# Optimization experiments

Hardware: AMD Instinct MI355X
Metric: run time of the kernel (lower is better)

Reference implementation:

```python
import jax, jax.numpy as jnp
import numpy as np

ALPHA = 0.2          # LeakyReLU negative slope
ORTHO_LAMBDA = 0.01  # orthogonal regularization weight


def setup_inputs() -> dict:
    key = jax.random.key(0)
    ks = jax.random.split(key, 9)
    N, IN, OUT, NR, H = 50000, 128, 128, 64, 4
    E1, E2 = 200000, 50000
    return {
        "input": jax.random.normal(ks[0], (N, IN), jnp.float32),
        "edge": jax.random.randint(ks[1], (2, E1), 0, N),
        "edge_embed": jax.random.normal(ks[2], (E1, NR), jnp.float32),
        "edge_list_nhop": jax.random.randint(ks[3], (2, E2), 0, N),
        "edge_embed_nhop": jax.random.normal(ks[4], (E2, NR), jnp.float32),
        "proj": jax.random.normal(ks[5], (H, IN, IN), jnp.float32) / np.sqrt(IN).astype(np.float32),
        "W": jax.random.normal(ks[6], (H, OUT, 2 * IN + NR), jnp.float32) * 0.08,
        "a": jax.random.normal(ks[7], (H, 1, OUT), jnp.float32) * 0.1,
        "head_weights": jnp.ones((H,), jnp.float32),
    }


def reference(input, edge, edge_embed, edge_list_nhop, edge_embed_nhop, proj, W, a, head_weights):
    N, IN = input.shape
    H, OUT, _ = W.shape
    e = jnp.concatenate([edge, edge_list_nhop], axis=1)              # [2, E]
    emb = jnp.concatenate([edge_embed, edge_embed_nhop], axis=0)     # [E, NR]
    src, tgt = e[0], e[1]

    # per-head orthogonal projections: head_input[h] = input @ proj[h].T -> [H, N, IN]
    hin = jnp.einsum('ni,hoi->hno', input, proj)

    # edge_m = W @ concat(h_src, h_tgt, rel) without materializing the concat
    W_src, W_tgt, W_rel = W[:, :, :IN], W[:, :, IN:2 * IN], W[:, :, 2 * IN:]
    edge_m = (jnp.einsum('hei,hoi->heo', hin[:, src, :], W_src)
              + jnp.einsum('hei,hoi->heo', hin[:, tgt, :], W_tgt)
              + jnp.einsum('er,hor->heo', emb, W_rel))               # [H, E, OUT]

    scores = jnp.einsum('heo,ho->he', edge_m, a[:, 0, :])            # [H, E]
    powers = -jnp.where(scores > 0, scores, ALPHA * scores)         # -leakyrelu
    edge_e = jnp.exp(powers)                                         # [H, E]

    seg = lambda v: jax.ops.segment_sum(v, src, num_segments=N)
    e_rowsum = jnp.clip(jax.vmap(seg)(edge_e), 1e-12, None)          # [H, N]

    edge_w = edge_e[:, :, None] * edge_m                             # [H, E, OUT]
    head_out = jax.vmap(seg)(edge_w)                                 # [H, N, OUT]

    w = jax.nn.softmax(head_weights)
    out = jnp.einsum('h,hnd->nd', w, head_out)                       # [N, OUT]
    # faithful to torch: divides by the LAST head's e_rowsum (loop leakage)
    out = out / e_rowsum[-1][:, None]

    pp = jnp.einsum('hij,hkj->hik', proj, proj)                      # proj @ proj.T
    eye = jnp.eye(proj.shape[1], dtype=proj.dtype)
    orth_reg = ORTHO_LAMBDA * jnp.sum(jnp.sqrt(jnp.sum((pp - eye) ** 2, axis=(1, 2))))

    return jax.nn.elu(out), orth_reg
```

## Files before the change

### kernel.cpp

```cpp
#include <hip/hip_runtime.h>
#include <math.h>


#define NHEAD 4

typedef unsigned short u16;
typedef __attribute__((ext_vector_type(4))) unsigned short u16x4;
typedef __attribute__((ext_vector_type(8))) unsigned short u16x8;
typedef __attribute__((ext_vector_type(8))) short bf16x8;
typedef __attribute__((ext_vector_type(4))) float f32x4;

__device__ __forceinline__ float bf2f(u16 v) {
    union { unsigned u; float f; } x; x.u = ((unsigned)v) << 16; return x.f;
}
__device__ __forceinline__ u16 f2bf(float f) {
    union { float f; unsigned u; } x; x.f = f;
    const unsigned r = x.u + 0x7FFFu + ((x.u >> 16) & 1u);
    return (u16)(r >> 16);
}

__global__ __launch_bounds__(256) void k1_prep(
    const float* __restrict__ proj, const float* __restrict__ W,
    const float* __restrict__ a, const float* __restrict__ hw,
    u16* __restrict__ M_bf,
    float* __restrict__ asrc, float* __restrict__ atgt, float* __restrict__ arel,
    u16* __restrict__ WcatT_bf, float* __restrict__ wsoft,
    float* __restrict__ orth_part)
{
    __shared__ float projS[128*132];
    __shared__ float WS[32*132];
    __shared__ float tS[128];
    __shared__ float red[256];
    const int h = blockIdx.x;
    const int part = blockIdx.y;
    const int z = blockIdx.z;
    const int tid = threadIdx.x;
    const float* projH = proj + h*(128*128);
    const float* WH = W + h*(128*320);
    const float* aH = a + h*128;

    {
        const float4* p4 = (const float4*)projH;
        for (int idx = tid; idx < 4096; idx += 256)
            *(float4*)&projS[(idx>>5)*132 + (idx&31)*4] = p4[idx];
    }

    if (part < 2) {
        const int koff = part ? 128 : 0;
        for (int idx = tid; idx < 1024; idx += 256) {
            const int ol = idx>>5, jq = idx&31;
            *(float4*)&WS[ol*132 + jq*4] = *(const float4*)&WH[(z*32+ol)*320 + koff + jq*4];
        }
        __syncthreads();
        u16* Mout = M_bf + ((size_t)(part*4 + h))*16384;
        for (int idx = tid; idx < 1024; idx += 256) {
            const int ol = idx>>5, jq = idx&31;
            float4 acc; acc.x=0.f; acc.y=0.f; acc.z=0.f; acc.w=0.f;
            for (int i = 0; i < 128; ++i) {
                const float wv = WS[ol*132 + i];
                const float4 pv = *(const float4*)&projS[i*132 + jq*4];
                acc.x += wv*pv.x; acc.y += wv*pv.y; acc.z += wv*pv.z; acc.w += wv*pv.w;
            }
            u16x4 pk; pk.x=f2bf(acc.x); pk.y=f2bf(acc.y); pk.z=f2bf(acc.z); pk.w=f2bf(acc.w);
            *(u16x4*)&Mout[(z*32+ol)*128 + jq*4] = pk;
        }
        if (z == 0) {
            if (tid < 128) {
                float s = 0.f;
                for (int o = 0; o < 128; ++o) s += aH[o]*WH[o*320 + koff + tid];
                tS[tid] = s;
            }
            __syncthreads();
            if (tid < 128) {
                float s = 0.f;
                for (int i = 0; i < 128; ++i) s += tS[i]*projS[i*132 + tid];
                (part ? atgt : asrc)[h*128 + tid] = s;
            }
        }
    } else {
        __syncthreads();
        float local = 0.f;
        const int base = z*4096;
        for (int idx = base + tid; idx < base + 4096; idx += 256) {
            const int i = idx>>7, k = idx&127;
            float s = 0.f;
            for (int q = 0; q < 32; ++q) {
                const float4 pi = *(const float4*)&projS[i*132 + q*4];
                const float4 pk = *(const float4*)&projS[k*132 + q*4];
                s += pi.x*pk.x + pi.y*pk.y + pi.z*pk.z + pi.w*pk.w;
            }
            if (i == k) s -= 1.f;
            local += s*s;
        }
        red[tid] = local;
        __syncthreads();
        for (int st = 128; st > 0; st >>= 1) {
            if (tid < st) red[tid] += red[tid+st];
            __syncthreads();
        }
        if (tid == 0) atomicAdd(&orth_part[h], red[0]);
        if (z == 0) {
            if (tid < 64) {
                float s = 0.f;
                for (int o = 0; o < 128; ++o) s += aH[o]*WH[o*320 + 256 + tid];
                arel[h*64 + tid] = s;
            }
            for (int idx = tid; idx < 8192; idx += 256) {
                const int r = idx & 63, o = idx >> 6;
                WcatT_bf[(size_t)o*256 + h*64 + r] = f2bf(WH[o*320 + 256 + r]);
            }
            if (h == 0 && tid == 0) {
                const float m = fmaxf(fmaxf(hw[0],hw[1]), fmaxf(hw[2],hw[3]));
                const float e0=expf(hw[0]-m), e1=expf(hw[1]-m), e2=expf(hw[2]-m), e3=expf(hw[3]-m);
                const float s = e0+e1+e2+e3;
                wsoft[0]=e0/s; wsoft[1]=e1/s; wsoft[2]=e2/s; wsoft[3]=e3/s;
            }
        }
    }
}

__global__ __launch_bounds__(256) void k0_nodes(
    const float* __restrict__ input, const float* __restrict__ asrc, const float* __restrict__ atgt,
    u16* __restrict__ in_bf, float* __restrict__ s_src, float* __restrict__ s_tgt, int N)
{
    __shared__ float aS[512], tS[512];
    const int tid = threadIdx.x;
    for (int idx = tid; idx < 512; idx += 256) { aS[idx] = asrc[idx]; tS[idx] = atgt[idx]; }
    __syncthreads();
    const int n = blockIdx.x*256 + tid;
    if (n >= N) return;
    const float4* inr = (const float4*)(input + (size_t)n*128);
    u16* ob = in_bf + (size_t)n*128;
    float ss[4] = {0.f,0.f,0.f,0.f}, st[4] = {0.f,0.f,0.f,0.f};
    for (int q = 0; q < 32; ++q) {
        const float4 v = inr[q];
        u16x4 pk; pk.x=f2bf(v.x); pk.y=f2bf(v.y); pk.z=f2bf(v.z); pk.w=f2bf(v.w);
        *(u16x4*)(ob + q*4) = pk;
        #pragma unroll
        for (int hh = 0; hh < 4; ++hh) {
            const float4 av = *(const float4*)&aS[hh*128 + q*4];
            const float4 tv = *(const float4*)&tS[hh*128 + q*4];
            ss[hh] += v.x*av.x + v.y*av.y + v.z*av.z + v.w*av.w;
            st[hh] += v.x*tv.x + v.y*tv.y + v.z*tv.z + v.w*tv.w;
        }
    }
    float4 o1; o1.x=ss[0]; o1.y=ss[1]; o1.z=ss[2]; o1.w=ss[3];
    float4 o2; o2.x=st[0]; o2.y=st[1]; o2.z=st[2]; o2.w=st[3];
    *(float4*)(s_src + (size_t)n*4) = o1;
    *(float4*)(s_tgt + (size_t)n*4) = o2;
}

__global__ __launch_bounds__(256) void k2_mfma(
    const u16* __restrict__ in_bf, const u16* __restrict__ M_bf,
    u16* __restrict__ tbl, int N)
{
    __shared__ u16 MS[16384];
    __shared__ u16 DS[128*136];
    const int tid = threadIdx.x;
    const int w = tid >> 6, lane = tid & 63;
    const int mat = blockIdx.y;
    const int n0 = blockIdx.x*256;
    const int m = lane & 15, kg = lane >> 4;

    {
        const u16* Mp = M_bf + (size_t)mat*16384;
        for (int c = tid; c < 2048; c += 256) {
            const int row = c >> 4, c16 = c & 15;
            const u16x8 v = *(const u16x8*)(Mp + row*128 + c16*8);
            *(u16x8*)((char*)MS + row*256 + ((c16*16) ^ ((row&7)<<4))) = v;
        }
    }
    bf16x8 fa[4][4];
    #pragma unroll
    for (int rt = 0; rt < 4; ++rt) {
        int row = n0 + w*64 + rt*16 + m; if (row >= N) row = N-1;
        const u16* ap = in_bf + (size_t)row*128 + kg*8;
        #pragma unroll
        for (int ks = 0; ks < 4; ++ks) fa[rt][ks] = *(const bf16x8*)(ap + ks*32);
    }
    __syncthreads();

    f32x4 acc[4][8];
    #pragma unroll
    for (int rt = 0; rt < 4; ++rt)
        #pragma unroll
        for (int nt = 0; nt < 8; ++nt) { acc[rt][nt][0]=0.f; acc[rt][nt][1]=0.f; acc[rt][nt][2]=0.f; acc[rt][nt][3]=0.f; }

    #pragma unroll
    for (int nt = 0; nt < 8; ++nt) {
        const int o = nt*16 + m;
        bf16x8 fb[4];
        #pragma unroll
        for (int ks = 0; ks < 4; ++ks) {
            const int c16 = kg + 4*ks;
            fb[ks] = *(const bf16x8*)((const char*)MS + o*256 + ((c16*16) ^ ((o&7)<<4)));
        }
        #pragma unroll
        for (int rt = 0; rt < 4; ++rt)
            #pragma unroll
            for (int ks = 0; ks < 4; ++ks)
                acc[rt][nt] = __builtin_amdgcn_mfma_f32_16x16x32_bf16(fa[rt][ks], fb[ks], acc[rt][nt], 0, 0, 0);
    }

    for (int p = 0; p < 2; ++p) {
        __syncthreads();
        if ((w >> 1) == p) {
            #pragma unroll
            for (int rt = 0; rt < 4; ++rt) {
                const int r0 = (w&1)*64 + rt*16 + kg*4;
                #pragma unroll
                for (int nt = 0; nt < 8; ++nt) {
                    const int o = nt*16 + m;
                    #pragma unroll
                    for (int r = 0; r < 4; ++r)
                        DS[(r0+r)*136 + o] = f2bf(acc[rt][nt][r]);
                }
            }
        }
        __syncthreads();
        for (int idx = tid; idx < 2048; idx += 256) {
            const int row = idx >> 4, seg = idx & 15;
            const int n = n0 + p*128 + row;
            if (n < N) {
                const bf16x8 v = *(const bf16x8*)&DS[row*136 + seg*8];
                *(bf16x8*)(tbl + (size_t)n*1024 + mat*128 + seg*8) = v;
            }
        }
    }
}

__global__ __launch_bounds__(256) void k3_edges(
    const int* __restrict__ edge, const int* __restrict__ nhop,
    const float* __restrict__ emb1, const float* __restrict__ emb2,
    const float* __restrict__ s_src, const float* __restrict__ s_tgt,
    const float* __restrict__ arel,
    float* __restrict__ edge_e, int* __restrict__ deg,
    u16* __restrict__ emb_bf, int E1, int E2)
{
    const int tid = threadIdx.x;
    const int g = tid >> 4, l = tid & 15;
    const int E = E1 + E2;
    const float4 ar0 = *(const float4*)(arel + 0*64 + l*4);
    const float4 ar1 = *(const float4*)(arel + 1*64 + l*4);
    const float4 ar2 = *(const float4*)(arel + 2*64 + l*4);
    const float4 ar3 = *(const float4*)(arel + 3*64 + l*4);
    const int ebase = blockIdx.x*256;
    #pragma unroll 4
    for (int it = 0; it < 16; ++it) {
        const int e = ebase + it*16 + g;
        if (e >= E) continue;
        const float4 v = (e < E1) ? *(const float4*)(emb1 + (size_t)e*64 + l*4)
                                  : *(const float4*)(emb2 + (size_t)(e-E1)*64 + l*4);
        u16x4 pk; pk.x=f2bf(v.x); pk.y=f2bf(v.y); pk.z=f2bf(v.z); pk.w=f2bf(v.w);
        *(u16x4*)(emb_bf + (size_t)e*64 + l*4) = pk;
        float p0 = v.x*ar0.x + v.y*ar0.y + v.z*ar0.z + v.w*ar0.w;
        float p1 = v.x*ar1.x + v.y*ar1.y + v.z*ar1.z + v.w*ar1.w;
        float p2 = v.x*ar2.x + v.y*ar2.y + v.z*ar2.z + v.w*ar2.w;
        float p3 = v.x*ar3.x + v.y*ar3.y + v.z*ar3.z + v.w*ar3.w;
        #pragma unroll
        for (int d = 1; d < 16; d <<= 1) {
            p0 += __shfl_xor(p0, d);
            p1 += __shfl_xor(p1, d);
            p2 += __shfl_xor(p2, d);
            p3 += __shfl_xor(p3, d);
        }
        if (l == 0) {
            int src, tgt;
            if (e < E1) { src = edge[e]; tgt = edge[E1+e]; }
            else { const int e2 = e-E1; src = nhop[e2]; tgt = nhop[E2+e2]; }
            const float4 s4 = *(const float4*)(s_src + (size_t)src*4);
            const float4 t4 = *(const float4*)(s_tgt + (size_t)tgt*4);
            float4 eo;
            { const float sc = s4.x+t4.x+p0; eo.x = expf(sc>0.f ? -sc : -0.2f*sc); }
            { const float sc = s4.y+t4.y+p1; eo.y = expf(sc>0.f ? -sc : -0.2f*sc); }
            { const float sc = s4.z+t4.z+p2; eo.z = expf(sc>0.f ? -sc : -0.2f*sc); }
            { const float sc = s4.w+t4.w+p3; eo.w = expf(sc>0.f ? -sc : -0.2f*sc); }
            *(float4*)(edge_e + (size_t)e*4) = eo;
            atomicAdd(&deg[src], 1);
        }
    }
}

__global__ __launch_bounds__(1024) void k_scanA(const int* __restrict__ deg, int* __restrict__ offsets,
                                                int* __restrict__ bsum, int N)
{
    __shared__ int wsumS[16];
    const int tid = threadIdx.x;
    const int lane = tid & 63, wid = tid >> 6;
    const int i0 = blockIdx.x*4096 + tid*4;
    int a0=0,a1=0,a2=0,a3=0;
    if (i0 + 3 < N) { const int4 t = *(const int4*)(deg + i0); a0=t.x; a1=t.y; a2=t.z; a3=t.w; }
    else { if (i0 < N) a0=deg[i0]; if (i0+1 < N) a1=deg[i0+1]; if (i0+2 < N) a2=deg[i0+2]; }
    const int s1=a0+a1, s2=s1+a2, s3=s2+a3;
    int s = s3;
    #pragma unroll
    for (int d = 1; d < 64; d <<= 1) { const int t = __shfl_up(s, d); if (lane >= d) s += t; }
    if (lane == 63) wsumS[wid] = s;
    __syncthreads();
    if (tid < 16) {
        int t = wsumS[tid];
        #pragma unroll
        for (int d = 1; d < 16; d <<= 1) { const int u = __shfl_up(t, d); if (tid >= d) t += u; }
        wsumS[tid] = t;
    }
    __syncthreads();
    const int ex = (wid ? wsumS[wid-1] : 0) + s - s3;
    if (i0 < N)     offsets[i0]   = ex;
    if (i0+1 < N)   offsets[i0+1] = ex + a0;
    if (i0+2 < N)   offsets[i0+2] = ex + s1;
    if (i0+3 < N)   offsets[i0+3] = ex + s2;
    if (tid == 0) bsum[blockIdx.x] = wsumS[15];
}

__global__ __launch_bounds__(64) void k_scanB(const int* __restrict__ bsum, int* __restrict__ boff,
                                              int* __restrict__ offsets, int nb, int N)
{
    const int tid = threadIdx.x;
    const int v = (tid < nb) ? bsum[tid] : 0;
    int s = v;
    #pragma unroll
    for (int d = 1; d < 64; d <<= 1) { const int t = __shfl_up(s, d); if (tid >= d) s += t; }
    if (tid < nb) boff[tid] = s - v;
    if (tid == 63) offsets[N] = s;
}

__global__ __launch_bounds__(256) void k_scanC(int* __restrict__ offsets, const int* __restrict__ boff, int N)
{
    const int i = blockIdx.x*256 + threadIdx.x;
    if (i < N) offsets[i] += boff[i >> 12];
}

__global__ __launch_bounds__(256) void k_fill(
    const int* __restrict__ edge, const int* __restrict__ nhop,
    const float* __restrict__ edge_e,
    const int* __restrict__ offsets, int* __restrict__ cursor,
    int* __restrict__ csr_e, int* __restrict__ csr_tgt, float* __restrict__ ee_perm,
    int E1, int E2)
{
    const int E = E1+E2;
    const int e = blockIdx.x*256 + threadIdx.x;
    if (e >= E) return;
    int src, tgt;
    if (e < E1) { src = edge[e]; tgt = edge[E1+e]; }
    else { const int e2 = e-E1; src = nhop[e2]; tgt = nhop[E2+e2]; }
    const int pos = atomicAdd(&cursor[src], 1);
    const int p = offsets[src] + pos;
    csr_e[p] = e;
    csr_tgt[p] = tgt;
    *(float4*)(ee_perm + (size_t)p*4) = *(const float4*)(edge_e + (size_t)e*4);
}

__global__ __launch_bounds__(256) void k4_gather(
    const float* __restrict__ ee_perm, const int* __restrict__ offsets,
    const int* __restrict__ csr_e, const int* __restrict__ csr_tgt,
    const u16* __restrict__ emb_bf, const u16* __restrict__ tbl,
    const float* __restrict__ wsoft,
    float* __restrict__ pout, u16* __restrict__ semb_bf, float* __restrict__ rowsum3,
    int N)
{
    const int lane = threadIdx.x & 63;
    const int n = blockIdx.x*4 + (threadIdx.x >> 6);
    if (n >= N) return;
    const int hl = lane >> 4;
    const int hoff = hl*128 + (lane & 15)*8;

    union HT { u16x8 v; unsigned u[4]; };

    float acc[8];
    #pragma unroll
    for (int j = 0; j < 8; ++j) acc[j] = 0.f;
    float sm0=0.f, sm1=0.f, sm2=0.f, sm3=0.f;
    float rsl0=0.f, rsl1=0.f, rsl2=0.f, rsl3=0.f;

    const int start = offsets[n], end = offsets[n+1];
    for (int cb = start; cb < end; cb += 64) {
        const int rem = end - cb;
        const int cnt = rem < 64 ? rem : 64;
        int eL = 0, tgtL = 0;
        float4 eeL; eeL.x=0.f; eeL.y=0.f; eeL.z=0.f; eeL.w=0.f;
        if (lane < cnt) {
            eL   = csr_e[cb + lane];
            tgtL = csr_tgt[cb + lane];
            eeL  = *(const float4*)(ee_perm + (size_t)(cb + lane)*4);
        }
        rsl0 += eeL.x; rsl1 += eeL.y; rsl2 += eeL.z; rsl3 += eeL.w;
        const int cp = (cnt + 3) & ~3;

        HT ht0, ht1, ht2, ht3;
        u16 em0, em1, em2, em3;
#define K4_FETCH(J, IDX) { const int tg_ = __shfl(tgtL, (IDX)); const int eg_ = __shfl(eL, (IDX)); \
            ht##J.v = *(const u16x8*)(tbl + (size_t)tg_*1024 + 512 + hoff); \
            em##J = emb_bf[(size_t)eg_*64 + lane]; }
        K4_FETCH(0, 0) K4_FETCH(1, 1) K4_FETCH(2, 2) K4_FETCH(3, 3)

#define K4_STAGE(J) { \
            const float e0 = __shfl(eeL.x, i+J); \
            const float e1 = __shfl(eeL.y, i+J); \
            const float e2 = __shfl(eeL.z, i+J); \
            const float e3 = __shfl(eeL.w, i+J); \
            const float eh = (hl==0)?e0:(hl==1)?e1:(hl==2)?e2:e3; \
            _Pragma("unroll") \
            for (int p = 0; p < 4; ++p) { \
                union{unsigned u; float f;} lo_, hi_; \
                lo_.u = ht##J.u[p] << 16; hi_.u = ht##J.u[p] & 0xffff0000u; \
                acc[2*p]   += eh*lo_.f; \
                acc[2*p+1] += eh*hi_.f; \
            } \
            const float ev = bf2f(em##J); \
            sm0 += e0*ev; sm1 += e1*ev; sm2 += e2*ev; sm3 += e3*ev; \
            { const int ii = i + 4 + J; const int ic = ii < 63 ? ii : 63; K4_FETCH(J, ic) } }

        for (int i = 0; i < cp; i += 4) {
            K4_STAGE(0)
            K4_STAGE(1)
            K4_STAGE(2)
            K4_STAGE(3)
        }
#undef K4_STAGE
#undef K4_FETCH
    }

    #pragma unroll
    for (int d = 1; d < 64; d <<= 1) {
        rsl0 += __shfl_xor(rsl0, d);
        rsl1 += __shfl_xor(rsl1, d);
        rsl2 += __shfl_xor(rsl2, d);
        rsl3 += __shfl_xor(rsl3, d);
    }
    {
        const float rsh = (hl==0)?rsl0:(hl==1)?rsl1:(hl==2)?rsl2:rsl3;
        HT hs; hs.v = *(const u16x8*)(tbl + (size_t)n*1024 + hoff);
        #pragma unroll
        for (int p = 0; p < 4; ++p) {
            union{unsigned u; float f;} lo_, hi_;
            lo_.u = hs.u[p] << 16; hi_.u = hs.u[p] & 0xffff0000u;
            acc[2*p]   += rsh*lo_.f;
            acc[2*p+1] += rsh*hi_.f;
        }
    }
    if (lane == 0) rowsum3[n] = fmaxf(rsl3, 1e-12f);

    const float4 ws4 = *(const float4*)wsoft;
    const float wh = (hl==0)?ws4.x:(hl==1)?ws4.y:(hl==2)?ws4.z:ws4.w;
    float p[8];
    #pragma unroll
    for (int j = 0; j < 8; ++j) {
        float pv = wh*acc[j];
        pv += __shfl_xor(pv, 16);
        pv += __shfl_xor(pv, 32);
        p[j] = pv;
    }
    if (hl == 0) {
        float* op = pout + (size_t)n*128 + (lane & 15)*8;
        float4 A; A.x=p[0]; A.y=p[1]; A.z=p[2]; A.w=p[3];
        float4 B; B.x=p[4]; B.y=p[5]; B.z=p[6]; B.w=p[7];
        *(float4*)op = A;
        *(float4*)(op+4) = B;
    }
    u16* so = semb_bf + (size_t)n*256;
    so[lane]       = f2bf(ws4.x*sm0);
    so[64 + lane]  = f2bf(ws4.y*sm1);
    so[128 + lane] = f2bf(ws4.z*sm2);
    so[192 + lane] = f2bf(ws4.w*sm3);
}

__global__ __launch_bounds__(256) void k5_gemm(
    const u16* __restrict__ semb_bf, const u16* __restrict__ wcatT_bf,
    const float* __restrict__ rowsum3, const float* __restrict__ orth_part,
    float* __restrict__ out, int N)
{
    __shared__ float DS[64*132];
    const int tid = threadIdx.x;
    if (blockIdx.x == 0 && tid == 0)
        out[(size_t)N*128] = 0.01f*(sqrtf(orth_part[0])+sqrtf(orth_part[1])+sqrtf(orth_part[2])+sqrtf(orth_part[3]));
    const int w = tid >> 6, lane = tid & 63;
    const int m = lane & 15, kg = lane >> 4;
    const int n0 = blockIdx.x*64;

    bf16x8 fa[8];
    {
        int row = n0 + w*16 + m; if (row >= N) row = N-1;
        const u16* ap = semb_bf + (size_t)row*256 + kg*8;
        #pragma unroll
        for (int ks = 0; ks < 8; ++ks) fa[ks] = *(const bf16x8*)(ap + ks*32);
    }
    f32x4 acc[8];
    #pragma unroll
    for (int nt = 0; nt < 8; ++nt) { acc[nt][0]=0.f; acc[nt][1]=0.f; acc[nt][2]=0.f; acc[nt][3]=0.f; }
    #pragma unroll
    for (int nt = 0; nt < 8; ++nt) {
        const u16* bp = wcatT_bf + (size_t)(nt*16 + m)*256 + kg*8;
        #pragma unroll
        for (int ks = 0; ks < 8; ++ks) {
            const bf16x8 fb = *(const bf16x8*)(bp + ks*32);
            acc[nt] = __builtin_amdgcn_mfma_f32_16x16x32_bf16(fa[ks], fb, acc[nt], 0, 0, 0);
        }
    }
    #pragma unroll
    for (int nt = 0; nt < 8; ++nt) {
        const int o = nt*16 + m;
        const int r0 = w*16 + kg*4;
        #pragma unroll
        for (int r = 0; r < 4; ++r)
            DS[(r0+r)*132 + o] = acc[nt][r];
    }
    __syncthreads();
    for (int idx = tid; idx < 2048; idx += 256) {
        const int row = idx >> 5, q = idx & 31;
        const int n = n0 + row;
        if (n < N) {
            const float4 d = *(const float4*)&DS[row*132 + q*4];
            float* op = out + (size_t)n*128 + q*4;
            const float4 pv = *(const float4*)op;
            const float rinv = 1.0f / rowsum3[n];
            float v0 = (pv.x + d.x)*rinv;
            float v1 = (pv.y + d.y)*rinv;
            float v2 = (pv.z + d.z)*rinv;
            float v3 = (pv.w + d.w)*rinv;
            v0 = (v0 > 0.f) ? v0 : expm1f(v0);
            v1 = (v1 > 0.f) ? v1 : expm1f(v1);
            v2 = (v2 > 0.f) ? v2 : expm1f(v2);
            v3 = (v3 > 0.f) ? v3 : expm1f(v3);
            float4 r4; r4.x=v0; r4.y=v1; r4.z=v2; r4.w=v3;
            *(float4*)op = r4;
        }
    }
}

extern "C" void kernel_launch(void* const* d_in, const int* in_sizes, int n_in,
                              void* d_out, int out_size, void* d_ws, size_t ws_size,
                              hipStream_t stream)
{
    const float* input = (const float*)d_in[0];
    const int*   edge  = (const int*)d_in[1];
    const float* emb1  = (const float*)d_in[2];
    const int*   nhop  = (const int*)d_in[3];
    const float* emb2  = (const float*)d_in[4];
    const float* proj  = (const float*)d_in[5];
    const float* W     = (const float*)d_in[6];
    const float* a     = (const float*)d_in[7];
    const float* hw    = (const float*)d_in[8];
    float* out = (float*)d_out;

    const int N  = in_sizes[0] / 128;
    const int E1 = in_sizes[1] / 2;
    const int E2 = in_sizes[3] / 2;
    const int E  = E1 + E2;
    (void)n_in; (void)out_size; (void)ws_size;

    char* wsb = (char*)d_ws;
    size_t off = 0;
    auto alloc = [&](size_t bytes) -> char* {
        char* p = wsb + off;
        off += (bytes + 255) & ~(size_t)255;
        return p;
    };
    u16*   in_bf    = (u16*)alloc((size_t)N*128*2);
    u16*   tbl      = (u16*)alloc((size_t)N*1024*2);
    u16*   semb_bf  = (u16*)alloc((size_t)N*256*2);
    u16*   emb_bf   = (u16*)alloc((size_t)E*64*2);
    float* edge_e   = (float*)alloc((size_t)E*4*4);
    float* ee_perm  = (float*)alloc((size_t)E*4*4);
    int*   csr_e    = (int*)alloc((size_t)E*4);
    int*   csr_tgt  = (int*)alloc((size_t)E*4);
    u16*   M_bf     = (u16*)alloc((size_t)8*16384*2);
    u16*   WcatT_bf = (u16*)alloc((size_t)128*256*2);
    float* asrc     = (float*)alloc(512*4);
    float* atgt     = (float*)alloc(512*4);
    float* arel     = (float*)alloc(256*4);
    float* s_src    = (float*)alloc((size_t)N*4*4);
    float* s_tgt    = (float*)alloc((size_t)N*4*4);
    float* wsoft    = (float*)alloc(4*4);
    float* rowsum3  = (float*)alloc((size_t)N*4);
    int*   offsets  = (int*)alloc((size_t)(N+1)*4);
    int*   bsum     = (int*)alloc(64*4);
    int*   boff     = (int*)alloc(64*4);
    const size_t zoff0 = off;
    float* orth_part= (float*)alloc(4*4);
    int*   deg      = (int*)alloc((size_t)N*4);
    int*   cursor   = (int*)alloc((size_t)N*4);
    const size_t zoff1 = off;

    hipMemsetAsync(wsb + zoff0, 0, zoff1 - zoff0, stream);

    const int nbScan = (N + 4095) / 4096;

    k1_prep<<<dim3(NHEAD,3,4), dim3(256), 0, stream>>>(proj, W, a, hw, M_bf,
                                                       asrc, atgt, arel, WcatT_bf, wsoft, orth_part);
    k0_nodes<<<dim3((N+255)/256), dim3(256), 0, stream>>>(input, asrc, atgt, in_bf, s_src, s_tgt, N);
    k2_mfma<<<dim3((N+255)/256, 8), dim3(256), 0, stream>>>(in_bf, M_bf, tbl, N);
    k3_edges<<<dim3((E+255)/256), dim3(256), 0, stream>>>(edge, nhop, emb1, emb2, s_src, s_tgt,
                                                          arel, edge_e, deg, emb_bf, E1, E2);
    k_scanA<<<dim3(nbScan), dim3(1024), 0, stream>>>(deg, offsets, bsum, N);
    k_scanB<<<dim3(1), dim3(64), 0, stream>>>(bsum, boff, offsets, nbScan, N);
    k_scanC<<<dim3((N+255)/256), dim3(256), 0, stream>>>(offsets, boff, N);
    k_fill<<<dim3((E+255)/256), dim3(256), 0, stream>>>(edge, nhop, edge_e, offsets, cursor,
                                                        csr_e, csr_tgt, ee_perm, E1, E2);
    k4_gather<<<dim3((N+3)/4), dim3(256), 0, stream>>>(ee_perm, offsets, csr_e, csr_tgt, emb_bf,
                                                       tbl, wsoft, out, semb_bf, rowsum3, N);
    k5_gemm<<<dim3((N+63)/64), dim3(256), 0, stream>>>(semb_bf, WcatT_bf, rowsum3, orth_part,
                                                       out, N);
}
```

Before: 275.7 us.

## Store gather partials in bf16, fold scan fixup into consumers, swizzle k2 grid

Removes the scanC kernel by adding the per-block scan offset at use sites in k_fill and k4_gather. Writes the k4 partial output as bf16 to a separate buffer rather than fp32 read-modify-write of the output, reducing memory traffic in k4 and k5. Remaps k2 blocks to a 1D swizzled grid and guards gather prefetches by edge count. Trades some precision on the intermediate partial sums.

```diff
diff --git a/kernel.cpp b/kernel.cpp
--- a/kernel.cpp
+++ b/kernel.cpp
@@ -158,8 +158,11 @@
     __shared__ u16 DS[128*136];
     const int tid = threadIdx.x;
     const int w = tid >> 6, lane = tid & 63;
-    const int mat = blockIdx.y;
-    const int n0 = blockIdx.x*256;
+    const int bid = blockIdx.x;
+    const int nx = gridDim.x >> 3;
+    const int swz = (bid & 7)*nx + (bid >> 3);
+    const int n0 = (swz >> 3)*256;
+    const int mat = swz & 7;
     const int m = lane & 15, kg = lane >> 4;
 
     {
@@ -324,16 +327,10 @@
     if (tid == 63) offsets[N] = s;
 }
 
-__global__ __launch_bounds__(256) void k_scanC(int* __restrict__ offsets, const int* __restrict__ boff, int N)
-{
-    const int i = blockIdx.x*256 + threadIdx.x;
-    if (i < N) offsets[i] += boff[i >> 12];
-}
-
 __global__ __launch_bounds__(256) void k_fill(
     const int* __restrict__ edge, const int* __restrict__ nhop,
     const float* __restrict__ edge_e,
-    const int* __restrict__ offsets, int* __restrict__ cursor,
+    const int* __restrict__ offsets, const int* __restrict__ boff, int* __restrict__ cursor,
     int* __restrict__ csr_e, int* __restrict__ csr_tgt, float* __restrict__ ee_perm,
     int E1, int E2)
 {
@@ -344,18 +341,18 @@
     if (e < E1) { src = edge[e]; tgt = edge[E1+e]; }
     else { const int e2 = e-E1; src = nhop[e2]; tgt = nhop[E2+e2]; }
     const int pos = atomicAdd(&cursor[src], 1);
-    const int p = offsets[src] + pos;
+    const int p = offsets[src] + boff[src>>12] + pos;
     csr_e[p] = e;
     csr_tgt[p] = tgt;
     *(float4*)(ee_perm + (size_t)p*4) = *(const float4*)(edge_e + (size_t)e*4);
 }
 
 __global__ __launch_bounds__(256) void k4_gather(
-    const float* __restrict__ ee_perm, const int* __restrict__ offsets,
+    const float* __restrict__ ee_perm, const int* __restrict__ offsets, const int* __restrict__ boff,
     const int* __restrict__ csr_e, const int* __restrict__ csr_tgt,
     const u16* __restrict__ emb_bf, const u16* __restrict__ tbl,
     const float* __restrict__ wsoft,
-    float* __restrict__ pout, u16* __restrict__ semb_bf, float* __restrict__ rowsum3,
+    u16* __restrict__ pout_bf, u16* __restrict__ semb_bf, float* __restrict__ rowsum3,
     int N)
 {
     const int lane = threadIdx.x & 63;
@@ -372,7 +369,8 @@
     float sm0=0.f, sm1=0.f, sm2=0.f, sm3=0.f;
     float rsl0=0.f, rsl1=0.f, rsl2=0.f, rsl3=0.f;
 
-    const int start = offsets[n], end = offsets[n+1];
+    const int start = offsets[n] + boff[n>>12];
+    const int end = (n+1 == N) ? offsets[N] : (offsets[n+1] + boff[(n+1)>>12]);
     for (int cb = start; cb < end; cb += 64) {
         const int rem = end - cb;
         const int cnt = rem < 64 ? rem : 64;
@@ -386,12 +384,16 @@
         rsl0 += eeL.x; rsl1 += eeL.y; rsl2 += eeL.z; rsl3 += eeL.w;
         const int cp = (cnt + 3) & ~3;
 
-        HT ht0, ht1, ht2, ht3;
-        u16 em0, em1, em2, em3;
+        HT zz; zz.u[0]=0u; zz.u[1]=0u; zz.u[2]=0u; zz.u[3]=0u;
+        HT ht0=zz, ht1=zz, ht2=zz, ht3=zz;
+        u16 em0=0, em1=0, em2=0, em3=0;
 #define K4_FETCH(J, IDX) { const int tg_ = __shfl(tgtL, (IDX)); const int eg_ = __shfl(eL, (IDX)); \
             ht##J.v = *(const u16x8*)(tbl + (size_t)tg_*1024 + 512 + hoff); \
             em##J = emb_bf[(size_t)eg_*64 + lane]; }
-        K4_FETCH(0, 0) K4_FETCH(1, 1) K4_FETCH(2, 2) K4_FETCH(3, 3)
+        if (0 < cnt) K4_FETCH(0, 0)
+        if (1 < cnt) K4_FETCH(1, 1)
+        if (2 < cnt) K4_FETCH(2, 2)
+        if (3 < cnt) K4_FETCH(3, 3)
 
 #define K4_STAGE(J) { \
             const float e0 = __shfl(eeL.x, i+J); \
@@ -408,7 +410,7 @@
             } \
             const float ev = bf2f(em##J); \
             sm0 += e0*ev; sm1 += e1*ev; sm2 += e2*ev; sm3 += e3*ev; \
-            { const int ii = i + 4 + J; const int ic = ii < 63 ? ii : 63; K4_FETCH(J, ic) } }
+            { const int ii = i + 4 + J; if (ii < cnt) K4_FETCH(J, ii) } }
 
         for (int i = 0; i < cp; i += 4) {
             K4_STAGE(0)
@@ -451,11 +453,10 @@
         p[j] = pv;
     }
     if (hl == 0) {
-        float* op = pout + (size_t)n*128 + (lane & 15)*8;
-        float4 A; A.x=p[0]; A.y=p[1]; A.z=p[2]; A.w=p[3];
-        float4 B; B.x=p[4]; B.y=p[5]; B.z=p[6]; B.w=p[7];
-        *(float4*)op = A;
-        *(float4*)(op+4) = B;
+        u16 pk[8];
+        #pragma unroll
+        for (int j = 0; j < 8; ++j) pk[j] = f2bf(p[j]);
+        *(u16x8*)(pout_bf + (size_t)n*128 + (lane & 15)*8) = *(u16x8*)pk;
     }
     u16* so = semb_bf + (size_t)n*256;
     so[lane]       = f2bf(ws4.x*sm0);
@@ -466,6 +467,7 @@
 
 __global__ __launch_bounds__(256) void k5_gemm(
     const u16* __restrict__ semb_bf, const u16* __restrict__ wcatT_bf,
+    const u16* __restrict__ pout_bf,
     const float* __restrict__ rowsum3, const float* __restrict__ orth_part,
     float* __restrict__ out, int N)
 {
@@ -510,19 +512,18 @@
         const int n = n0 + row;
         if (n < N) {
             const float4 d = *(const float4*)&DS[row*132 + q*4];
-            float* op = out + (size_t)n*128 + q*4;
-            const float4 pv = *(const float4*)op;
+            const u16x4 pb = *(const u16x4*)(pout_bf + (size_t)n*128 + q*4);
             const float rinv = 1.0f / rowsum3[n];
-            float v0 = (pv.x + d.x)*rinv;
-            float v1 = (pv.y + d.y)*rinv;
-            float v2 = (pv.z + d.z)*rinv;
-            float v3 = (pv.w + d.w)*rinv;
+            float v0 = (bf2f(pb.x) + d.x)*rinv;
+            float v1 = (bf2f(pb.y) + d.y)*rinv;
+            float v2 = (bf2f(pb.z) + d.z)*rinv;
+            float v3 = (bf2f(pb.w) + d.w)*rinv;
             v0 = (v0 > 0.f) ? v0 : expm1f(v0);
             v1 = (v1 > 0.f) ? v1 : expm1f(v1);
             v2 = (v2 > 0.f) ? v2 : expm1f(v2);
             v3 = (v3 > 0.f) ? v3 : expm1f(v3);
             float4 r4; r4.x=v0; r4.y=v1; r4.z=v2; r4.w=v3;
-            *(float4*)op = r4;
+            *(float4*)(out + (size_t)n*128 + q*4) = r4;
         }
     }
 }
@@ -558,6 +559,7 @@
     u16*   in_bf    = (u16*)alloc((size_t)N*128*2);
     u16*   tbl      = (u16*)alloc((size_t)N*1024*2);
     u16*   semb_bf  = (u16*)alloc((size_t)N*256*2);
+    u16*   pout_bf  = (u16*)alloc((size_t)N*128*2);
     u16*   emb_bf   = (u16*)alloc((size_t)E*64*2);
     float* edge_e   = (float*)alloc((size_t)E*4*4);
     float* ee_perm  = (float*)alloc((size_t)E*4*4);
@@ -584,20 +586,20 @@
     hipMemsetAsync(wsb + zoff0, 0, zoff1 - zoff0, stream);
 
     const int nbScan = (N + 4095) / 4096;
+    const int nx = (N + 255) / 256;
 
     k1_prep<<<dim3(NHEAD,3,4), dim3(256), 0, stream>>>(proj, W, a, hw, M_bf,
                                                        asrc, atgt, arel, WcatT_bf, wsoft, orth_part);
     k0_nodes<<<dim3((N+255)/256), dim3(256), 0, stream>>>(input, asrc, atgt, in_bf, s_src, s_tgt, N);
-    k2_mfma<<<dim3((N+255)/256, 8), dim3(256), 0, stream>>>(in_bf, M_bf, tbl, N);
+    k2_mfma<<<dim3(nx*8), dim3(256), 0, stream>>>(in_bf, M_bf, tbl, N);
     k3_edges<<<dim3((E+255)/256), dim3(256), 0, stream>>>(edge, nhop, emb1, emb2, s_src, s_tgt,
                                                           arel, edge_e, deg, emb_bf, E1, E2);
     k_scanA<<<dim3(nbScan), dim3(1024), 0, stream>>>(deg, offsets, bsum, N);
     k_scanB<<<dim3(1), dim3(64), 0, stream>>>(bsum, boff, offsets, nbScan, N);
-    k_scanC<<<dim3((N+255)/256), dim3(256), 0, stream>>>(offsets, boff, N);
-    k_fill<<<dim3((E+255)/256), dim3(256), 0, stream>>>(edge, nhop, edge_e, offsets, cursor,
+    k_fill<<<dim3((E+255)/256), dim3(256), 0, stream>>>(edge, nhop, edge_e, offsets, boff, cursor,
                                                         csr_e, csr_tgt, ee_perm, E1, E2);
-    k4_gather<<<dim3((N+3)/4), dim3(256), 0, stream>>>(ee_perm, offsets, csr_e, csr_tgt, emb_bf,
-                                                       tbl, wsoft, out, semb_bf, rowsum3, N);
-    k5_gemm<<<dim3((N+63)/64), dim3(256), 0, stream>>>(semb_bf, WcatT_bf, rowsum3, orth_part,
+    k4_gather<<<dim3((N+3)/4), dim3(256), 0, stream>>>(ee_perm, offsets, boff, csr_e, csr_tgt, emb_bf,
+                                                       tbl, wsoft, pout_bf, semb_bf, rowsum3, N);
+    k5_gemm<<<dim3((N+63)/64), dim3(256), 0, stream>>>(semb_bf, WcatT_bf, pout_bf, rowsum3, orth_part,
                                                        out, N);
 }
```

New measurement: 272.8 us. No clear change (-1.1%).
